# Kernel optimization log

Hardware: AMD Instinct MI355X
Metric: run time of the kernel (lower is better)

Reference implementation:

```python
import jax, jax.numpy as jnp
import numpy as np

N_NODES = 100000
N_EDGES = 1600000
VOCAB = 50000
F_DIM = 128
N_GRAPHS = 64
N_LABELS = 20


def setup_inputs() -> dict:
    key = jax.random.key(0)
    ks = jax.random.split(key, 12)
    s = 1.0 / np.sqrt(F_DIM)
    inp = {
        "x": jax.random.randint(ks[0], (N_NODES,), 0, VOCAB),
        "edge_index": jax.random.randint(ks[1], (2, N_EDGES), 0, N_NODES),
        "batch": jnp.sort(jax.random.randint(ks[2], (N_NODES,), 0, N_GRAPHS)),
        "emb": jax.random.normal(ks[3], (VOCAB, F_DIM), jnp.float32),
        "w1_rel": jax.random.normal(ks[4], (F_DIM, F_DIM), jnp.float32) * s,
        "w1_root": jax.random.normal(ks[5], (F_DIM, F_DIM), jnp.float32) * s,
        "b1": jnp.zeros((F_DIM,), jnp.float32),
        "w2_rel": jax.random.normal(ks[6], (F_DIM, F_DIM), jnp.float32) * s,
        "w2_root": jax.random.normal(ks[7], (F_DIM, F_DIM), jnp.float32) * s,
        "b2": jnp.zeros((F_DIM,), jnp.float32),
        "lw1": jax.random.normal(ks[8], (2 * F_DIM, 128), jnp.float32) * (1.0 / np.sqrt(2 * F_DIM)),
        "lb1": jnp.zeros((128,), jnp.float32),
        "lw2": jax.random.normal(ks[9], (128, 64), jnp.float32) * (1.0 / np.sqrt(128)),
        "lb2": jnp.zeros((64,), jnp.float32),
        "lw3": jax.random.normal(ks[10], (64, N_LABELS), jnp.float32) * (1.0 / np.sqrt(64)),
        "lb3": jnp.zeros((N_LABELS,), jnp.float32),
    }
    return inp


def graph_conv(h, src, dst, w_rel, w_root, b):
    # PyG GraphConv (aggr='add'): out_i = W_rel @ sum_{j->i} h_j + b + W_root @ h_i
    agg = jax.ops.segment_sum(h[src], dst, num_segments=N_NODES)  # [N, F]
    return agg @ w_rel + b + h @ w_root


def reference(x, edge_index, batch, emb, w1_rel, w1_root, b1,
              w2_rel, w2_root, b2, lw1, lb1, lw2, lb2, lw3, lb3):
    src, dst = edge_index[0], edge_index[1]
    h = emb[x]                                              # [N, F]
    h = jax.nn.relu(graph_conv(h, src, dst, w1_rel, w1_root, b1))
    h = jax.nn.relu(graph_conv(h, src, dst, w2_rel, w2_root, b2))
    # global max pool + global mean pool per graph
    gmax = jax.ops.segment_max(h, batch, num_segments=N_GRAPHS)  # [G, F]
    gsum = jax.ops.segment_sum(h, batch, num_segments=N_GRAPHS)
    counts = jax.ops.segment_sum(jnp.ones((N_NODES,), h.dtype), batch,
                                 num_segments=N_GRAPHS)
    gmean = gsum / jnp.maximum(counts, 1.0)[:, None]
    g = jnp.concatenate([gmax, gmean], axis=1)              # [G, 2F]
    g = jax.nn.relu(g @ lw1 + lb1)
    g = jax.nn.relu(g @ lw2 + lb2)
    # NOTE: original applies log_softmax over dim=0 (the graph dim) - kept faithful
    return jax.nn.log_softmax(g @ lw3 + lb3, axis=0)
```

## Files before the change

### kernel.cpp

```cpp
#include <hip/hip_runtime.h>
#include <hip/hip_bf16.h>

#define N_NODES   100000
#define N_EDGES   1600000
#define N_GRAPHS  64
#define FDIM      128
#define N_LABELS  20
#define NBK       64
#define P_BKT     1563
#define NCHUNKS   512
#define NCHUNKS_LOG 9
#define CHUNK     3125
#define SCAN_M    (P_BKT * NCHUNKS)
#define SB1_BLOCKS 3126
#define SB_BLOCKS 391
#define BPITCH    136

typedef __bf16 bf16x8 __attribute__((ext_vector_type(8)));
typedef float  f32x4  __attribute__((ext_vector_type(4)));
union frag_u { uint4 u; bf16x8 b; };

__device__ __forceinline__ unsigned bfr(float v) {
  unsigned b = __float_as_uint(v);
  return (b + 0x7fffu + ((b >> 16) & 1u)) >> 16;
}

__global__ __launch_bounds__(256) void prep_kernel(
    const float* __restrict__ emb, unsigned short* __restrict__ embbf,
    const float* __restrict__ w1rel, const float* __restrict__ w1rt,
    const float* __restrict__ w2rel, const float* __restrict__ w2rt,
    unsigned short* __restrict__ wt1, unsigned short* __restrict__ wt2,
    const int* __restrict__ batch, int* __restrict__ start,
    float* __restrict__ pool, float* __restrict__ zrow,
    int* __restrict__ csr, int* __restrict__ csr2,
    int* __restrict__ offsets) {
  int b = blockIdx.x;
  int tid = threadIdx.x;
  if (b < 6250) {
    int i = b * 256 + tid;
    float4 v = ((const float4*)emb)[i];
    uint2 o;
    o.x = bfr(v.x) | (bfr(v.y) << 16);
    o.y = bfr(v.z) | (bfr(v.w) << 16);
    ((uint2*)embbf)[i] = o;
  } else if (b < 6506) {
    int gid = (b - 6250) * 256 + tid;
    int l = gid >> 15;
    int rem = gid & 32767;
    int c = rem >> 8, k = rem & 255;
    const float* w = l ? ((k < 128) ? w2rel : w2rt) : ((k < 128) ? w1rel : w1rt);
    float v = w[(size_t)(k & 127) * FDIM + c];
    (l ? wt2 : wt1)[c * 256 + k] = (unsigned short)bfr(v);
  } else if (b < 6897) {
    int i = (b - 6506) * 256 + tid;
    if (i >= N_NODES) return;
    int bb = batch[i];
    int bp = (i == 0) ? -1 : batch[i - 1];
    for (int g = bp + 1; g <= bb; ++g) start[g] = i;
    if (i == N_NODES - 1) {
      for (int g = bb + 1; g <= N_GRAPHS; ++g) start[g] = N_NODES;
    }
  } else {
    int i = (b - 6897) * 256 + tid;
    if (i < N_GRAPHS * 256) pool[i] = 0.f;
    if (i < FDIM) zrow[i] = 0.f;
    if (i < 32) { csr[N_EDGES + i] = 0; csr2[N_EDGES + i] = 0; }
    if (i == 32) offsets[N_NODES] = N_EDGES;
  }
}

__global__ __launch_bounds__(256) void histA_kernel(
    const int* __restrict__ ei, int* __restrict__ cntmat) {
  __shared__ int hist[P_BKT];
  int tid = threadIdx.x;
  for (int i = tid; i < P_BKT; i += 256) hist[i] = 0;
  __syncthreads();
  int base = blockIdx.x * CHUNK;
  for (int i = tid; i < CHUNK; i += 256) {
    int d = ei[N_EDGES + base + i];
    atomicAdd(&hist[d >> 6], 1);
  }
  __syncthreads();
  for (int p = tid; p < P_BKT; p += 256)
    cntmat[p * NCHUNKS + blockIdx.x] = hist[p];
}

__global__ __launch_bounds__(256) void scanB1_kernel(
    const int* __restrict__ v, int* __restrict__ part,
    int* __restrict__ bsum) {
  __shared__ int s[256];
  int tid = threadIdx.x;
  int i = blockIdx.x * 256 + tid;
  int val = (i < SCAN_M) ? v[i] : 0;
  s[tid] = val;
  __syncthreads();
  for (int off = 1; off < 256; off <<= 1) {
    int t = (tid >= off) ? s[tid - off] : 0;
    __syncthreads();
    s[tid] += t;
    __syncthreads();
  }
  if (i < SCAN_M) part[i] = s[tid] - val;
  if (tid == 255) bsum[blockIdx.x] = s[255];
}

__global__ __launch_bounds__(512) void scanB2_kernel(int* __restrict__ bsum) {
  __shared__ int s[512];
  int tid = threadIdx.x;
  int v[8];
  int tot = 0;
#pragma unroll
  for (int j = 0; j < 8; ++j) {
    int idx = tid * 8 + j;
    v[j] = (idx < SB1_BLOCKS) ? bsum[idx] : 0;
    tot += v[j];
  }
  s[tid] = tot;
  __syncthreads();
  for (int off = 1; off < 512; off <<= 1) {
    int t = (tid >= off) ? s[tid - off] : 0;
    __syncthreads();
    s[tid] += t;
    __syncthreads();
  }
  int run = s[tid] - tot;
#pragma unroll
  for (int j = 0; j < 8; ++j) {
    int idx = tid * 8 + j;
    int val = v[j];
    if (idx < SB1_BLOCKS) bsum[idx] = run;
    run += val;
  }
}

__global__ __launch_bounds__(256) void scanB3_kernel(
    int* __restrict__ part, const int* __restrict__ bsum,
    int* __restrict__ bstart) {
  int i = blockIdx.x * 256 + threadIdx.x;
  if (i < SCAN_M) {
    int o = part[i] + bsum[blockIdx.x];
    part[i] = o;
    if ((i & (NCHUNKS - 1)) == 0) bstart[i >> NCHUNKS_LOG] = o;
  }
  if (blockIdx.x == 0 && threadIdx.x == 0) bstart[P_BKT] = N_EDGES;
}

__global__ __launch_bounds__(256) void scatA_kernel(
    const int* __restrict__ ei, const int* __restrict__ S,
    int* __restrict__ ebuf) {
  __shared__ int rc[P_BKT];
  int tid = threadIdx.x;
  for (int p = tid; p < P_BKT; p += 256)
    rc[p] = S[p * NCHUNKS + blockIdx.x];
  __syncthreads();
  int base = blockIdx.x * CHUNK;
  for (int i = tid; i < CHUNK; i += 256) {
    int s0 = ei[base + i];
    int d0 = ei[N_EDGES + base + i];
    int pos = atomicAdd(&rc[d0 >> 6], 1);
    ebuf[pos] = (s0 << 6) | (d0 & 63);
  }
}

__global__ __launch_bounds__(256) void fill2_kernel(
    const int* __restrict__ ebuf, const int* __restrict__ bstart,
    const int* __restrict__ x, int* __restrict__ offsets,
    int* __restrict__ csr, int* __restrict__ csr2) {
  __shared__ int ldeg[NBK], loffs[NBK], rc2[NBK];
  int tid = threadIdx.x;
  int p = blockIdx.x;
  int beg = bstart[p], end = bstart[p + 1];
  if (tid < NBK) ldeg[tid] = 0;
  __syncthreads();
  for (int i = beg + tid; i < end; i += 256)
    atomicAdd(&ldeg[ebuf[i] & 63], 1);
  __syncthreads();
  if (tid == 0) {
    int run = 0;
    for (int r = 0; r < NBK; ++r) { loffs[r] = run; run += ldeg[r]; }
  }
  __syncthreads();
  if (tid < NBK) {
    rc2[tid] = loffs[tid];
    int gn = p * NBK + tid;
    if (gn < N_NODES) offsets[gn] = beg + loffs[tid];
  }
  __syncthreads();
  for (int i = beg + tid; i < end; i += 256) {
    int e = ebuf[i];
    int ld = e & 63;
    int src = e >> 6;
    int pos = atomicAdd(&rc2[ld], 1);
    csr[beg + pos] = src;
    csr2[beg + pos] = x[src];
  }
}

__global__ __launch_bounds__(256) void agg_kernel(
    const unsigned short* __restrict__ feat, const int* __restrict__ srcidx,
    const int* __restrict__ offs, const float* __restrict__ zrow,
    unsigned short* __restrict__ aggout) {
  int sub = threadIdx.x >> 4;
  int fq  = threadIdx.x & 15;
  int node = blockIdx.x * 16 + sub;

  float4 e0 = make_float4(0.f, 0.f, 0.f, 0.f);
  float4 e1 = make_float4(0.f, 0.f, 0.f, 0.f);
  float4 o0 = make_float4(0.f, 0.f, 0.f, 0.f);
  float4 o1 = make_float4(0.f, 0.f, 0.f, 0.f);
  int s = offs[node], e = offs[node + 1];

  const uint4* __restrict__ fb = (const uint4*)feat;
  const uint4* __restrict__ zb = (const uint4*)zrow;

  int p = s;
  for (; p + 8 <= e; p += 8) {
    const uint4* rp[8];
#pragma unroll
    for (int u = 0; u < 8; ++u)
      rp[u] = fb + (size_t)srcidx[p + u] * 16;
    uint4 w[8];
#pragma unroll
    for (int u = 0; u < 8; ++u) w[u] = rp[u][fq];
#pragma unroll
    for (int u = 0; u < 8; ++u) {
      float4& A = (u & 1) ? o0 : e0;
      float4& B = (u & 1) ? o1 : e1;
      A.x += __uint_as_float(w[u].x << 16);
      A.y += __uint_as_float(w[u].x & 0xffff0000u);
      A.z += __uint_as_float(w[u].y << 16);
      A.w += __uint_as_float(w[u].y & 0xffff0000u);
      B.x += __uint_as_float(w[u].z << 16);
      B.y += __uint_as_float(w[u].z & 0xffff0000u);
      B.z += __uint_as_float(w[u].w << 16);
      B.w += __uint_as_float(w[u].w & 0xffff0000u);
    }
  }
  if (p < e) {
    const uint4* rp[8];
#pragma unroll
    for (int u = 0; u < 8; ++u) {
      int iu = srcidx[p + u];
      rp[u] = (p + u < e) ? (fb + (size_t)iu * 16) : zb;
    }
    uint4 w[8];
#pragma unroll
    for (int u = 0; u < 8; ++u) w[u] = rp[u][fq];
#pragma unroll
    for (int u = 0; u < 8; ++u) {
      float4& A = (u & 1) ? o0 : e0;
      float4& B = (u & 1) ? o1 : e1;
      A.x += __uint_as_float(w[u].x << 16);
      A.y += __uint_as_float(w[u].x & 0xffff0000u);
      A.z += __uint_as_float(w[u].y << 16);
      A.w += __uint_as_float(w[u].y & 0xffff0000u);
      B.x += __uint_as_float(w[u].z << 16);
      B.y += __uint_as_float(w[u].z & 0xffff0000u);
      B.z += __uint_as_float(w[u].w << 16);
      B.w += __uint_as_float(w[u].w & 0xffff0000u);
    }
  }
  float f0 = e0.x + o0.x, f1 = e0.y + o0.y, f2 = e0.z + o0.z, f3 = e0.w + o0.w;
  float f4 = e1.x + o1.x, f5 = e1.y + o1.y, f6 = e1.z + o1.z, f7 = e1.w + o1.w;
  uint4 o;
  o.x = bfr(f0) | (bfr(f1) << 16);
  o.y = bfr(f2) | (bfr(f3) << 16);
  o.z = bfr(f4) | (bfr(f5) << 16);
  o.w = bfr(f6) | (bfr(f7) << 16);
  ((uint4*)aggout)[(size_t)node * 16 + fq] = o;
}

__global__ __launch_bounds__(256, 2) void gemm_kernel(
    const unsigned short* __restrict__ aggbf,
    const unsigned short* __restrict__ rootbf,
    const int* __restrict__ hidx,
    const unsigned short* __restrict__ wt,
    const float* __restrict__ bias,
    const int* __restrict__ batch,
    float* __restrict__ pool,
    unsigned short* __restrict__ hout_bf) {
  __shared__ unsigned short B_s[128 * BPITCH];
  int tid = threadIdx.x;
  int nodeBase = blockIdx.x * 128;
  int lane = tid & 63;
  int wv = tid >> 6;
  int wbase = wv * 32;
  int lo = lane & 15, hi = lane >> 4;

  int gnode[2], hroot[2];
#pragma unroll
  for (int mt = 0; mt < 2; ++mt) {
    int g = nodeBase + wbase + mt * 16 + lo;
    if (g > N_NODES - 1) g = N_NODES - 1;
    gnode[mt] = g;
    hroot[mt] = hidx ? hidx[g] : g;
  }

  frag_u afr[2][8];
#pragma unroll
  for (int mt = 0; mt < 2; ++mt) {
#pragma unroll
    for (int t = 0; t < 4; ++t)
      afr[mt][t].u =
          *(const uint4*)(aggbf + (size_t)gnode[mt] * FDIM + t * 32 + hi * 8);
#pragma unroll
    for (int t = 0; t < 4; ++t)
      afr[mt][4 + t].u =
          *(const uint4*)(rootbf + (size_t)hroot[mt] * FDIM + t * 32 + hi * 8);
  }

  f32x4 acc[2][8];
#pragma unroll
  for (int nt = 0; nt < 8; ++nt) {
    float b = bias[nt * 16 + lo];
#pragma unroll
    for (int mt = 0; mt < 2; ++mt) {
      acc[mt][nt][0] = b; acc[mt][nt][1] = b;
      acc[mt][nt][2] = b; acc[mt][nt][3] = b;
    }
  }

  int sr = tid >> 1;
  int so = (tid & 1) * 64;

#pragma unroll
  for (int h = 0; h < 2; ++h) {
    __syncthreads();
#pragma unroll
    for (int i = 0; i < 8; ++i)
      *(uint4*)(B_s + sr * BPITCH + so + i * 8) =
          *(const uint4*)(wt + sr * 256 + h * 128 + so + i * 8);
    __syncthreads();
#pragma unroll
    for (int tt = 0; tt < 4; ++tt) {
      frag_u bfv[8];
#pragma unroll
      for (int nt = 0; nt < 8; ++nt)
        bfv[nt].u =
            *(const uint4*)&B_s[(nt * 16 + lo) * BPITCH + tt * 32 + hi * 8];
#pragma unroll
      for (int mt = 0; mt < 2; ++mt)
#pragma unroll
        for (int nt = 0; nt < 8; ++nt)
          acc[mt][nt] = __builtin_amdgcn_mfma_f32_16x16x32_bf16(
              afr[mt][h * 4 + tt].b, bfv[nt].b, acc[mt][nt], 0, 0, 0);
    }
  }

  if (hout_bf) {
#pragma unroll
    for (int mt = 0; mt < 2; ++mt) {
#pragma unroll
      for (int r = 0; r < 4; ++r) {
        int n = nodeBase + wbase + mt * 16 + hi * 4 + r;
        if (n < N_NODES) {
          unsigned short* o = hout_bf + (size_t)n * FDIM + lo;
#pragma unroll
          for (int nt = 0; nt < 8; ++nt)
            o[nt * 16] = (unsigned short)bfr(fmaxf(acc[mt][nt][r], 0.f));
        }
      }
    }
  } else {
#pragma unroll
    for (int mt = 0; mt < 2; ++mt)
#pragma unroll
      for (int nt = 0; nt < 8; ++nt)
#pragma unroll
        for (int r = 0; r < 4; ++r)
          acc[mt][nt][r] = fmaxf(acc[mt][nt][r], 0.f);

#pragma unroll
    for (int mt = 0; mt < 2; ++mt) {
      int rowBase = nodeBase + wbase + mt * 16;
      int lastRow = rowBase + 15;
      int gF = batch[rowBase < N_NODES ? rowBase : N_NODES - 1];
      int gL = batch[lastRow < N_NODES ? lastRow : N_NODES - 1];
      if (gF == gL && lastRow < N_NODES) {
#pragma unroll
        for (int nt = 0; nt < 8; ++nt) {
          float mx = fmaxf(fmaxf(acc[mt][nt][0], acc[mt][nt][1]),
                           fmaxf(acc[mt][nt][2], acc[mt][nt][3]));
          float sm = acc[mt][nt][0] + acc[mt][nt][1] +
                     acc[mt][nt][2] + acc[mt][nt][3];
          mx = fmaxf(mx, __shfl_xor(mx, 16));
          sm += __shfl_xor(sm, 16);
          mx = fmaxf(mx, __shfl_xor(mx, 32));
          sm += __shfl_xor(sm, 32);
          if (hi == 0) {
            int c = nt * 16 + lo;
            atomicMax((unsigned int*)&pool[gF * 256 + c], __float_as_uint(mx));
            atomicAdd(&pool[gF * 256 + 128 + c], sm);
          }
        }
      } else {
#pragma unroll
        for (int r = 0; r < 4; ++r) {
          int n = rowBase + hi * 4 + r;
          if (n < N_NODES) {
            int g = batch[n];
#pragma unroll
            for (int nt = 0; nt < 8; ++nt) {
              int c = nt * 16 + lo;
              atomicMax((unsigned int*)&pool[g * 256 + c],
                        __float_as_uint(acc[mt][nt][r]));
              atomicAdd(&pool[g * 256 + 128 + c], acc[mt][nt][r]);
            }
          }
        }
      }
    }
  }
}

__global__ void head1_kernel(const float* __restrict__ pool,
                             const int* __restrict__ start,
                             const float* __restrict__ lw1,
                             const float* __restrict__ lb1,
                             float* __restrict__ t1) {
  int gid = blockIdx.x * 256 + threadIdx.x;
  int r = gid >> 7, c = gid & 127;
  int cnt = start[r + 1] - start[r];
  float inv = 1.f / (float)(cnt > 1 ? cnt : 1);
  float a0 = 0.f, a1 = 0.f;
  for (int k = 0; k < 128; ++k) a0 += pool[r * 256 + k] * lw1[k * 128 + c];
  for (int k = 0; k < 128; ++k)
    a1 += pool[r * 256 + 128 + k] * lw1[(128 + k) * 128 + c];
  t1[gid] = fmaxf(lb1[c] + a0 + a1 * inv, 0.f);
}

__global__ void head2_kernel(const float* __restrict__ t1,
                             const float* __restrict__ lw2,
                             const float* __restrict__ lb2,
                             float* __restrict__ t2) {
  int gid = blockIdx.x * 256 + threadIdx.x;
  int r = gid >> 6, c = gid & 63;
  float acc = lb2[c];
  for (int k = 0; k < 128; ++k) acc += t1[r * 128 + k] * lw2[k * 64 + c];
  t2[gid] = fmaxf(acc, 0.f);
}

__global__ __launch_bounds__(256) void head3_kernel(
    const float* __restrict__ t2, const float* __restrict__ lw3,
    const float* __restrict__ lb3, float* __restrict__ out) {
  __shared__ float lg[N_GRAPHS * N_LABELS];
  __shared__ float col[N_LABELS];
  int tid = threadIdx.x;
  for (int o = tid; o < N_GRAPHS * N_LABELS; o += 256) {
    int r = o / N_LABELS, c = o - r * N_LABELS;
    float acc = lb3[c];
    for (int k = 0; k < 64; ++k) acc += t2[r * 64 + k] * lw3[k * N_LABELS + c];
    lg[o] = acc;
  }
  __syncthreads();
  if (tid < N_LABELS) {
    float m = -1e30f;
    for (int r = 0; r < N_GRAPHS; ++r) m = fmaxf(m, lg[r * N_LABELS + tid]);
    float s = 0.f;
    for (int r = 0; r < N_GRAPHS; ++r) s += expf(lg[r * N_LABELS + tid] - m);
    col[tid] = m + logf(s);
  }
  __syncthreads();
  for (int o = tid; o < N_GRAPHS * N_LABELS; o += 256) {
    int c = o % N_LABELS;
    out[o] = lg[o] - col[c];
  }
}

extern "C" void kernel_launch(void* const* d_in, const int* in_sizes, int n_in,
                              void* d_out, int out_size, void* d_ws, size_t ws_size,
                              hipStream_t stream) {
  const int*   x     = (const int*)  d_in[0];
  const int*   ei    = (const int*)  d_in[1];
  const int*   batch = (const int*)  d_in[2];
  const float* emb   = (const float*)d_in[3];
  const float* w1rel = (const float*)d_in[4];
  const float* w1rt  = (const float*)d_in[5];
  const float* b1    = (const float*)d_in[6];
  const float* w2rel = (const float*)d_in[7];
  const float* w2rt  = (const float*)d_in[8];
  const float* b2    = (const float*)d_in[9];
  const float* lw1   = (const float*)d_in[10];
  const float* lb1   = (const float*)d_in[11];
  const float* lw2   = (const float*)d_in[12];
  const float* lb2   = (const float*)d_in[13];
  const float* lw3   = (const float*)d_in[14];
  const float* lb3   = (const float*)d_in[15];
  float* out = (float*)d_out;

  char* ws = (char*)d_ws;
  const size_t HB   = 51200000;
  const size_t CSRB = 6400128;
  const size_t OFFB = 400128;
  unsigned short* embbf = (unsigned short*)(ws);
  int*   cntmat  = (int*)  (ws + 13000000);
  int*   S       = (int*)  (ws + 16500000);
  int*   bsum    = (int*)  (ws + 20000000);
  unsigned short* aggbf = (unsigned short*)(ws + HB);
  int*   ebuf    = (int*)  (ws + HB);
  int*   csr     = (int*)  (ws + 2 * HB);
  int*   csr2    = (int*)  (ws + 2 * HB + CSRB);
  int*   offsets = (int*)  (ws + 2 * HB + 2 * CSRB);
  int*   bstart  = (int*)  (ws + 2 * HB + 2 * CSRB + OFFB);
  float* zrow    = (float*)(ws + 2 * HB + 2 * CSRB + OFFB + 6400);
  int*   start   = (int*)  (ws + 2 * HB + 2 * CSRB + OFFB + 6912);
  float* pool    = (float*)(ws + 2 * HB + 2 * CSRB + OFFB + 7424);
  float* t1      = (float*)(ws + 2 * HB + 2 * CSRB + OFFB + 72960);
  float* t2      = (float*)(ws + 2 * HB + 2 * CSRB + OFFB + 105728);
  unsigned short* hbf =
      (unsigned short*)(ws + 2 * HB + 2 * CSRB + OFFB + 122112);
  unsigned short* wt1 =
      (unsigned short*)(ws + 2 * HB + 2 * CSRB + OFFB + 122112 + 25600000);
  unsigned short* wt2 = wt1 + 128 * 256;

  prep_kernel<<<6961, 256, 0, stream>>>(emb, embbf, w1rel, w1rt, w2rel, w2rt,
                                        wt1, wt2, batch, start, pool, zrow,
                                        csr, csr2, offsets);

  histA_kernel<<<NCHUNKS, 256, 0, stream>>>(ei, cntmat);
  scanB1_kernel<<<SB1_BLOCKS, 256, 0, stream>>>(cntmat, S, bsum);
  scanB2_kernel<<<1, 512, 0, stream>>>(bsum);
  scanB3_kernel<<<SB1_BLOCKS, 256, 0, stream>>>(S, bsum, bstart);
  scatA_kernel<<<NCHUNKS, 256, 0, stream>>>(ei, S, ebuf);
  fill2_kernel<<<P_BKT, 256, 0, stream>>>(ebuf, bstart, x, offsets, csr, csr2);

  agg_kernel<<<N_NODES / 16, 256, 0, stream>>>(embbf, csr2, offsets, zrow, aggbf);
  gemm_kernel<<<(N_NODES + 127) / 128, 256, 0, stream>>>(
      aggbf, embbf, x, wt1, b1, (const int*)nullptr, (float*)nullptr, hbf);

  agg_kernel<<<N_NODES / 16, 256, 0, stream>>>(hbf, csr, offsets, zrow, aggbf);
  gemm_kernel<<<(N_NODES + 127) / 128, 256, 0, stream>>>(
      aggbf, hbf, (const int*)nullptr, wt2, b2, batch, pool,
      (unsigned short*)nullptr);

  head1_kernel<<<32, 256, 0, stream>>>(pool, start, lw1, lb1, t1);
  head2_kernel<<<16, 256, 0, stream>>>(t1, lw2, lb2, t2);
  head3_kernel<<<1, 256, 0, stream>>>(t2, lw3, lb3, out);
}
```

Baseline: 371.1 us.

## Drop LDS weight staging in GEMM, read B fragments from global per wave

```diff
diff --git a/kernel.cpp b/kernel.cpp
--- a/kernel.cpp
+++ b/kernel.cpp
@@ -14,7 +14,6 @@
 #define SCAN_M    (P_BKT * NCHUNKS)
 #define SB1_BLOCKS 3126
 #define SB_BLOCKS 391
-#define BPITCH    136
 
 typedef __bf16 bf16x8 __attribute__((ext_vector_type(8)));
 typedef float  f32x4  __attribute__((ext_vector_type(4)));
@@ -270,7 +269,7 @@
   ((uint4*)aggout)[(size_t)node * 16 + fq] = o;
 }
 
-__global__ __launch_bounds__(256, 2) void gemm_kernel(
+__global__ __launch_bounds__(256, 4) void gemm_kernel(
     const unsigned short* __restrict__ aggbf,
     const unsigned short* __restrict__ rootbf,
     const int* __restrict__ hidx,
@@ -279,133 +278,91 @@
     const int* __restrict__ batch,
     float* __restrict__ pool,
     unsigned short* __restrict__ hout_bf) {
-  __shared__ unsigned short B_s[128 * BPITCH];
-  int tid = threadIdx.x;
-  int nodeBase = blockIdx.x * 128;
+  int tid = threadIdx.x;
   int lane = tid & 63;
   int wv = tid >> 6;
-  int wbase = wv * 32;
   int lo = lane & 15, hi = lane >> 4;
-
-  int gnode[2], hroot[2];
-#pragma unroll
-  for (int mt = 0; mt < 2; ++mt) {
-    int g = nodeBase + wbase + mt * 16 + lo;
-    if (g > N_NODES - 1) g = N_NODES - 1;
-    gnode[mt] = g;
-    hroot[mt] = hidx ? hidx[g] : g;
-  }
-
-  frag_u afr[2][8];
-#pragma unroll
-  for (int mt = 0; mt < 2; ++mt) {
-#pragma unroll
-    for (int t = 0; t < 4; ++t)
-      afr[mt][t].u =
-          *(const uint4*)(aggbf + (size_t)gnode[mt] * FDIM + t * 32 + hi * 8);
-#pragma unroll
-    for (int t = 0; t < 4; ++t)
-      afr[mt][4 + t].u =
-          *(const uint4*)(rootbf + (size_t)hroot[mt] * FDIM + t * 32 + hi * 8);
-  }
-
-  f32x4 acc[2][8];
+  int base = blockIdx.x * 64 + wv * 16;
+
+  int g = base + lo;
+  if (g > N_NODES - 1) g = N_NODES - 1;
+  int hr = hidx ? hidx[g] : g;
+
+  frag_u afr[8];
+#pragma unroll
+  for (int t = 0; t < 4; ++t)
+    afr[t].u = *(const uint4*)(aggbf + (size_t)g * FDIM + t * 32 + hi * 8);
+#pragma unroll
+  for (int t = 0; t < 4; ++t)
+    afr[4 + t].u = *(const uint4*)(rootbf + (size_t)hr * FDIM + t * 32 + hi * 8);
+
+  f32x4 acc[8];
 #pragma unroll
   for (int nt = 0; nt < 8; ++nt) {
     float b = bias[nt * 16 + lo];
-#pragma unroll
-    for (int mt = 0; mt < 2; ++mt) {
-      acc[mt][nt][0] = b; acc[mt][nt][1] = b;
-      acc[mt][nt][2] = b; acc[mt][nt][3] = b;
-    }
-  }
-
-  int sr = tid >> 1;
-  int so = (tid & 1) * 64;
-
-#pragma unroll
-  for (int h = 0; h < 2; ++h) {
-    __syncthreads();
-#pragma unroll
-    for (int i = 0; i < 8; ++i)
-      *(uint4*)(B_s + sr * BPITCH + so + i * 8) =
-          *(const uint4*)(wt + sr * 256 + h * 128 + so + i * 8);
-    __syncthreads();
-#pragma unroll
-    for (int tt = 0; tt < 4; ++tt) {
-      frag_u bfv[8];
-#pragma unroll
-      for (int nt = 0; nt < 8; ++nt)
-        bfv[nt].u =
-            *(const uint4*)&B_s[(nt * 16 + lo) * BPITCH + tt * 32 + hi * 8];
-#pragma unroll
-      for (int mt = 0; mt < 2; ++mt)
+    acc[nt][0] = b; acc[nt][1] = b; acc[nt][2] = b; acc[nt][3] = b;
+  }
+
+#pragma unroll
+  for (int kk = 0; kk < 8; ++kk) {
+#pragma unroll
+    for (int nt = 0; nt < 8; ++nt) {
+      frag_u bfv;
+      bfv.u = *(const uint4*)(wt + (size_t)(nt * 16 + lo) * 256 + kk * 32 + hi * 8);
+      acc[nt] = __builtin_amdgcn_mfma_f32_16x16x32_bf16(
+          afr[kk].b, bfv.b, acc[nt], 0, 0, 0);
+    }
+  }
+
+  if (hout_bf) {
+#pragma unroll
+    for (int r = 0; r < 4; ++r) {
+      int n = base + hi * 4 + r;
+      if (n < N_NODES) {
+        unsigned short* o = hout_bf + (size_t)n * FDIM + lo;
 #pragma unroll
         for (int nt = 0; nt < 8; ++nt)
-          acc[mt][nt] = __builtin_amdgcn_mfma_f32_16x16x32_bf16(
-              afr[mt][h * 4 + tt].b, bfv[nt].b, acc[mt][nt], 0, 0, 0);
-    }
-  }
-
-  if (hout_bf) {
-#pragma unroll
-    for (int mt = 0; mt < 2; ++mt) {
-#pragma unroll
-      for (int r = 0; r < 4; ++r) {
-        int n = nodeBase + wbase + mt * 16 + hi * 4 + r;
-        if (n < N_NODES) {
-          unsigned short* o = hout_bf + (size_t)n * FDIM + lo;
-#pragma unroll
-          for (int nt = 0; nt < 8; ++nt)
-            o[nt * 16] = (unsigned short)bfr(fmaxf(acc[mt][nt][r], 0.f));
+          o[nt * 16] = (unsigned short)bfr(fmaxf(acc[nt][r], 0.f));
+      }
+    }
+  } else {
+#pragma unroll
+    for (int nt = 0; nt < 8; ++nt)
+#pragma unroll
+      for (int r = 0; r < 4; ++r)
+        acc[nt][r] = fmaxf(acc[nt][r], 0.f);
+
+    int lastRow = base + 15;
+    int gF = batch[base < N_NODES ? base : N_NODES - 1];
+    int gL = batch[lastRow < N_NODES ? lastRow : N_NODES - 1];
+    if (gF == gL && lastRow < N_NODES) {
+#pragma unroll
+      for (int nt = 0; nt < 8; ++nt) {
+        float mx = fmaxf(fmaxf(acc[nt][0], acc[nt][1]),
+                         fmaxf(acc[nt][2], acc[nt][3]));
+        float sm = acc[nt][0] + acc[nt][1] + acc[nt][2] + acc[nt][3];
+        mx = fmaxf(mx, __shfl_xor(mx, 16));
+        sm += __shfl_xor(sm, 16);
+        mx = fmaxf(mx, __shfl_xor(mx, 32));
+        sm += __shfl_xor(sm, 32);
+        if (hi == 0) {
+          int c = nt * 16 + lo;
+          atomicMax((unsigned int*)&pool[gF * 256 + c], __float_as_uint(mx));
+          atomicAdd(&pool[gF * 256 + 128 + c], sm);
         }
       }
-    }
-  } else {
-#pragma unroll
-    for (int mt = 0; mt < 2; ++mt)
-#pragma unroll
-      for (int nt = 0; nt < 8; ++nt)
-#pragma unroll
-        for (int r = 0; r < 4; ++r)
-          acc[mt][nt][r] = fmaxf(acc[mt][nt][r], 0.f);
-
-#pragma unroll
-    for (int mt = 0; mt < 2; ++mt) {
-      int rowBase = nodeBase + wbase + mt * 16;
-      int lastRow = rowBase + 15;
-      int gF = batch[rowBase < N_NODES ? rowBase : N_NODES - 1];
-      int gL = batch[lastRow < N_NODES ? lastRow : N_NODES - 1];
-      if (gF == gL && lastRow < N_NODES) {
-#pragma unroll
-        for (int nt = 0; nt < 8; ++nt) {
-          float mx = fmaxf(fmaxf(acc[mt][nt][0], acc[mt][nt][1]),
-                           fmaxf(acc[mt][nt][2], acc[mt][nt][3]));
-          float sm = acc[mt][nt][0] + acc[mt][nt][1] +
-                     acc[mt][nt][2] + acc[mt][nt][3];
-          mx = fmaxf(mx, __shfl_xor(mx, 16));
-          sm += __shfl_xor(sm, 16);
-          mx = fmaxf(mx, __shfl_xor(mx, 32));
-          sm += __shfl_xor(sm, 32);
-          if (hi == 0) {
+    } else {
+#pragma unroll
+      for (int r = 0; r < 4; ++r) {
+        int n = base + hi * 4 + r;
+        if (n < N_NODES) {
+          int gg = batch[n];
+#pragma unroll
+          for (int nt = 0; nt < 8; ++nt) {
             int c = nt * 16 + lo;
-            atomicMax((unsigned int*)&pool[gF * 256 + c], __float_as_uint(mx));
-            atomicAdd(&pool[gF * 256 + 128 + c], sm);
-          }
-        }
-      } else {
-#pragma unroll
-        for (int r = 0; r < 4; ++r) {
-          int n = rowBase + hi * 4 + r;
-          if (n < N_NODES) {
-            int g = batch[n];
-#pragma unroll
-            for (int nt = 0; nt < 8; ++nt) {
-              int c = nt * 16 + lo;
-              atomicMax((unsigned int*)&pool[g * 256 + c],
-                        __float_as_uint(acc[mt][nt][r]));
-              atomicAdd(&pool[g * 256 + 128 + c], acc[mt][nt][r]);
-            }
+            atomicMax((unsigned int*)&pool[gg * 256 + c],
+                      __float_as_uint(acc[nt][r]));
+            atomicAdd(&pool[gg * 256 + 128 + c], acc[nt][r]);
           }
         }
       }
@@ -525,11 +482,11 @@
   fill2_kernel<<<P_BKT, 256, 0, stream>>>(ebuf, bstart, x, offsets, csr, csr2);
 
   agg_kernel<<<N_NODES / 16, 256, 0, stream>>>(embbf, csr2, offsets, zrow, aggbf);
-  gemm_kernel<<<(N_NODES + 127) / 128, 256, 0, stream>>>(
+  gemm_kernel<<<(N_NODES + 63) / 64, 256, 0, stream>>>(
       aggbf, embbf, x, wt1, b1, (const int*)nullptr, (float*)nullptr, hbf);
 
   agg_kernel<<<N_NODES / 16, 256, 0, stream>>>(hbf, csr, offsets, zrow, aggbf);
-  gemm_kernel<<<(N_NODES + 127) / 128, 256, 0, stream>>>(
+  gemm_kernel<<<(N_NODES + 63) / 64, 256, 0, stream>>>(
       aggbf, hbf, (const int*)nullptr, wt2, b2, batch, pool,
       (unsigned short*)nullptr);
 
```

Measured after the change: 436.1 us. +17.5%, slower.
